# Kernel tuning notes

Measured on AMD Instinct MI355X. Metric: run time of the kernel, lower is better.

Reference implementation:

```python
import jax, jax.numpy as jnp
import numpy as np

DT = 0.01          # oscillator integration step
GPI_TAU = 0.01     # gpi accumulation rate
NOISE_TAU = 1.0    # noise scale
MIN_OMEGA, MAX_OMEGA = 0.1, 1.0


def clinear(xr, xi, Wr, Wi, br, bi):
    # complex linear: (Wr + i Wi)(xr + i xi) + (br + i bi), weights stored [out, in]
    yr = xr @ Wr.T - xi @ Wi.T + br
    yi = xr @ Wi.T + xi @ Wr.T + bi
    return yr, yi


def crelu(yr, yi):
    # ReLU applied to real and imaginary parts independently
    return jax.nn.relu(yr), jax.nn.relu(yi)


def hopf_step(xr, xi, r, phi, omega):
    # Hopf oscillator in polar form, forced by complex input x = xr + i xi:
    #   dr   = dt * ( r(1 - r^2) + Re(x e^{-i phi}) )
    #   dphi = dt * ( omega + Im(x e^{-i phi}) / r )
    # output = r_new * e^{i phi_new}
    c, s = jnp.cos(phi), jnp.sin(phi)
    r_new = r + DT * (r * (1.0 - r * r) + xr * c + xi * s)
    phi_new = phi + DT * (omega + (xi * c - xr * s) / jnp.maximum(r, 1e-6))
    return r_new * jnp.cos(phi_new), r_new * jnp.sin(phi_new), r_new, phi_new


def setup_inputs() -> dict:
    T, D, U, A = 4096, 256, 2048, 64
    key = jax.random.key(0)
    ks = jax.random.split(key, 16)

    def lin(k, out_d, in_d):
        k1, k2, k3, k4 = jax.random.split(k, 4)
        sc = 1.0 / np.sqrt(in_d)
        return (jax.random.normal(k1, (out_d, in_d), dtype=jnp.float32) * sc,
                jax.random.normal(k2, (out_d, in_d), dtype=jnp.float32) * sc,
                jax.random.normal(k3, (out_d,), dtype=jnp.float32) * sc,
                jax.random.normal(k4, (out_d,), dtype=jnp.float32) * sc)

    l1Wr, l1Wi, l1br, l1bi = lin(ks[0], U, D)
    dpWr, dpWi, dpbr, dpbi = lin(ks[1], A, U)
    ipWr, ipWi, ipbr, ipbi = lin(ks[2], A, U)
    cWr, cWi, cbr, cbi = lin(ks[3], 1, U)
    return {
        'state': jax.random.normal(ks[4], (T, 1, D), dtype=jnp.float32),
        'phi1_init': jax.random.uniform(ks[5], (1, U), dtype=jnp.float32),
        'phi2_init': jax.random.uniform(ks[6], (1, U), dtype=jnp.float32),
        'noise_u': jax.random.uniform(ks[7], (T, A), dtype=jnp.float32),
        'omega1': jax.random.uniform(ks[8], (U,), minval=MIN_OMEGA, maxval=MAX_OMEGA, dtype=jnp.float32),
        'omega2': jax.random.uniform(ks[9], (U,), minval=MIN_OMEGA, maxval=MAX_OMEGA, dtype=jnp.float32),
        'l1Wr': l1Wr, 'l1Wi': l1Wi, 'l1br': l1br, 'l1bi': l1bi,
        'dpWr': dpWr, 'dpWi': dpWi, 'dpbr': dpbr, 'dpbi': dpbi,
        'ipWr': ipWr, 'ipWi': ipWi, 'ipbr': ipbr, 'ipbi': ipbi,
        'cWr': cWr, 'cWi': cWi, 'cbr': cbr, 'cbi': cbi,
    }


def reference(state, phi1_init, phi2_init, noise_u, omega1, omega2,
              l1Wr, l1Wi, l1br, l1bi, dpWr, dpWi, dpbr, dpbi,
              ipWr, ipWi, ipbr, ipbi, cWr, cWi, cbr, cbi):
    U = l1Wr.shape[0]
    A = dpWr.shape[0]
    carry0 = (jnp.ones((1, U)), phi1_init * 0.1,   # r1, phi1 (torch.rand/10)
              jnp.ones((1, U)), phi2_init * 0.1,   # r2, phi2
              jnp.zeros((1, A)),                   # gpi
              jnp.zeros((1, 1)))                   # p_value

    def step(carry, xs):
        r1, phi1, r2, phi2, gpi, p_value = carry
        s_t, nz_t = xs  # s_t: [1, D], nz_t: [A]
        # x = cReLU(l1(complex(state[t], state[t])))
        xr, xi = crelu(*clinear(s_t, s_t, l1Wr, l1Wi, l1br, l1bi))
        d1r, d1i, r1, phi1 = hopf_step(xr, xi, r1, phi1, omega1)
        d2r, d2i, r2, phi2 = hopf_step(xr, xi, r2, phi2, omega2)
        vr, vi = clinear(d1r, d1i, cWr, cWi, cbr, cbi)
        value = jnp.sqrt(vr * vr + vi * vi)          # |critic(d1out)|  [1,1]
        delta_V = value - p_value                    # pd_flag = sc_flag = 0
        lD1 = jax.nn.sigmoid(5.0 * delta_V)
        lD2 = jax.nn.sigmoid(-5.0 * delta_V)
        dpr, dpi = crelu(*clinear(d1r * lD1, d1i * lD1, dpWr, dpWi, dpbr, dpbi))
        ipr, ipi = crelu(*clinear(d2r * lD2, d2i * lD2, ipWr, ipWi, ipbr, ipbi))
        noise = NOISE_TAU * (nz_t[None, :] * 2.0 * lD2 - lD2)  # real-valued, adds to real part
        diff_r = dpr - (ipr + noise)
        diff_i = dpi - ipi
        gpi = gpi + GPI_TAU * jnp.sqrt(diff_r * diff_r + diff_i * diff_i)
        return (r1, phi1, r2, phi2, gpi, value), (gpi, value)

    (r1, phi1, r2, phi2, gpi, value), (gpi_traj, value_traj) = jax.lax.scan(
        step, carry0, (state, noise_u))
    probs = jax.nn.softmax(gpi, axis=1)
    return probs, value, gpi_traj
```

## Files before the change

kernel.cpp:

```cpp
#include <hip/hip_runtime.h>
#include <hip/hip_bf16.h>
#include <stdint.h>


#define T_ 4096
#define D_ 256
#define U_ 2048
#define A_ 64

__device__ __forceinline__ uint32_t pack2(float lo, float hi) {
  __hip_bfloat16 l = __float2bfloat16(lo);
  __hip_bfloat16 h = __float2bfloat16(hi);
  uint16_t lu, hu;
  __builtin_memcpy(&lu, &l, 2);
  __builtin_memcpy(&hu, &h, 2);
  return (uint32_t)lu | ((uint32_t)hu << 16);
}
__device__ __forceinline__ float bflo(uint32_t p) { return __uint_as_float(p << 16); }
__device__ __forceinline__ float bfhi(uint32_t p) { return __uint_as_float(p & 0xffff0000u); }

__global__ __launch_bounds__(256) void k_gemm1(
    const float* __restrict__ S, const float* __restrict__ Wr,
    const float* __restrict__ Wi, const float* __restrict__ br,
    const float* __restrict__ bi, float* __restrict__ xc) {
  __shared__ float sT[32][68];
  __shared__ float wrT[32][68];
  __shared__ float wiT[32][68];
  const int tid = threadIdx.x;
  const int t0 = blockIdx.x * 64;
  const int u0 = blockIdx.y * 64;
  const int un = tid & 15, tm = tid >> 4;
  const int lr = tid >> 3;
  const int lc = (tid & 7) * 4;
  float accR[4][4] = {}, accI[4][4] = {};
  for (int k0 = 0; k0 < D_; k0 += 32) {
    __syncthreads();
#pragma unroll
    for (int p = 0; p < 2; ++p) {
      const int row = p * 32 + lr;
      float4 v = *(const float4*)&S[(size_t)(t0 + row) * D_ + k0 + lc];
      sT[lc + 0][row] = v.x; sT[lc + 1][row] = v.y;
      sT[lc + 2][row] = v.z; sT[lc + 3][row] = v.w;
      float4 a = *(const float4*)&Wr[(size_t)(u0 + row) * D_ + k0 + lc];
      wrT[lc + 0][row] = a.x; wrT[lc + 1][row] = a.y;
      wrT[lc + 2][row] = a.z; wrT[lc + 3][row] = a.w;
      float4 b = *(const float4*)&Wi[(size_t)(u0 + row) * D_ + k0 + lc];
      wiT[lc + 0][row] = b.x; wiT[lc + 1][row] = b.y;
      wiT[lc + 2][row] = b.z; wiT[lc + 3][row] = b.w;
    }
    __syncthreads();
#pragma unroll
    for (int k = 0; k < 32; ++k) {
      const float4 sv = *(const float4*)&sT[k][tm * 4];
      const float4 ar = *(const float4*)&wrT[k][un * 4];
      const float4 ai = *(const float4*)&wiT[k][un * 4];
      const float ss[4] = {sv.x, sv.y, sv.z, sv.w};
      const float wd[4] = {ar.x - ai.x, ar.y - ai.y, ar.z - ai.z, ar.w - ai.w};
      const float wm[4] = {ar.x + ai.x, ar.y + ai.y, ar.z + ai.z, ar.w + ai.w};
#pragma unroll
      for (int i = 0; i < 4; ++i)
#pragma unroll
        for (int j = 0; j < 4; ++j) {
          accR[i][j] = fmaf(ss[i], wd[j], accR[i][j]);
          accI[i][j] = fmaf(ss[i], wm[j], accI[i][j]);
        }
    }
  }
  const float4 brv = *(const float4*)&br[u0 + un * 4];
  const float4 biv = *(const float4*)&bi[u0 + un * 4];
  const float brx[4] = {brv.x, brv.y, brv.z, brv.w};
  const float bix[4] = {biv.x, biv.y, biv.z, biv.w};
#pragma unroll
  for (int i = 0; i < 4; ++i) {
    float vr[4], vi[4];
#pragma unroll
    for (int j = 0; j < 4; ++j) {
      vr[j] = fmaxf(accR[i][j] + brx[j], 0.f);
      vi[j] = fmaxf(accI[i][j] + bix[j], 0.f);
    }
    const size_t base = ((size_t)(t0 + tm * 4 + i) * U_ + u0 + un * 4) * 2;
    *(float4*)&xc[base + 0] = make_float4(vr[0], vi[0], vr[1], vi[1]);
    *(float4*)&xc[base + 4] = make_float4(vr[2], vi[2], vr[3], vi[3]);
  }
}

#define HOPF_LOAD(BUF, i, tbase)                                            \
  do {                                                                      \
    const float* bx_ = xc + (size_t)((tbase) + (i)) * (U_ * 2);             \
    asm volatile("global_load_dwordx2 %0, %1, %2"                           \
                 : "=v"(BUF[i])                                             \
                 : "v"(voffx), "s"(bx_));                                   \
  } while (0)

#define HOPF_STEP(BUF, i, tb)                                               \
  do {                                                                      \
    const float xr_ = BUF[i].x, xi_ = BUF[i].y;                             \
    const float f_ = fmaf(xr_, c, xi_ * s);                                 \
    const float g_ = fmaf(xi_, c, -(xr_ * s));                              \
    const float rn_ = fmaf(0.01f, fmaf(r, fmaf(-r, r, 1.0f), f_), r);       \
    const float rinv_ = __builtin_amdgcn_rcpf(fmaxf(r, 1e-6f));             \
    const float phin_ = fmaf(0.01f, g_ * rinv_, phi + dto);                 \
    float cn_, sn_;                                                         \
    __sincosf(phin_, &sn_, &cn_);                                           \
    uint32_t pk_;                                                           \
    asm("v_cvt_pk_bf16_f32 %0, %1, %2"                                     \
        : "=v"(pk_)                                                         \
        : "v"(rn_ * cn_), "v"(rn_ * sn_));                                  \
    const uint32_t* bd_ = dst + (size_t)((tb) + (i)) * U_;                  \
    asm volatile("global_store_dword %0, %1, %2" ::"v"(voffd), "v"(pk_),    \
                 "s"(bd_));                                                  \
    r = rn_; phi = phin_; c = cn_; s = sn_;                                 \
  } while (0)

#define VMWAIT(N)                                  \
  asm volatile("s_waitcnt vmcnt(" #N ")");         \
  __builtin_amdgcn_sched_barrier(0)

__global__ __launch_bounds__(64, 1) void k_hopf(
    const float* __restrict__ xc, const float* __restrict__ phi1,
    const float* __restrict__ phi2, const float* __restrict__ om1,
    const float* __restrict__ om2, uint32_t* __restrict__ d1c,
    uint32_t* __restrict__ d2c) {
  const int ub = blockIdx.x & 31;
  const int osc = blockIdx.x >> 5;
  const int u = ub * 64 + threadIdx.x;
  float phi = (osc ? phi2[u] : phi1[u]) * 0.1f;
  const float omega = osc ? om2[u] : om1[u];
  const uint32_t* __restrict__ dst = (osc ? d2c : d1c);
  const float dto = 0.01f * omega;
  float r = 1.0f;
  float c, s;
  __sincosf(phi, &s, &c);
  const uint32_t voffx = (uint32_t)u * 8u;
  const uint32_t voffd = (uint32_t)u * 4u;

  constexpr int PF = 32;
  float2 bufA[PF], bufB[PF];
#pragma unroll
  for (int i = 0; i < PF; ++i) HOPF_LOAD(bufA, i, 0);
#pragma unroll
  for (int i = 0; i < PF; ++i) HOPF_LOAD(bufB, i, PF);
  VMWAIT(32);

  for (int t0 = 0; t0 < T_; t0 += 2 * PF) {
#pragma unroll
    for (int i = 0; i < PF; ++i) HOPF_STEP(bufA, i, t0);
    {
      int tp = t0 + 2 * PF;
      if (tp >= T_) tp = 0;
#pragma unroll
      for (int i = 0; i < PF; ++i) HOPF_LOAD(bufA, i, tp);
    }
    VMWAIT(63);
#pragma unroll
    for (int i = 0; i < PF; ++i) HOPF_STEP(bufB, i, t0 + PF);
    {
      int tp = t0 + 3 * PF;
      if (tp >= T_) tp = 0;
#pragma unroll
      for (int i = 0; i < PF; ++i) HOPF_LOAD(bufB, i, tp);
    }
    VMWAIT(63);
  }
  asm volatile("s_waitcnt vmcnt(0)");
}

__global__ __launch_bounds__(256) void k_critic(
    const uint32_t* __restrict__ d1c, const float* __restrict__ cWr,
    const float* __restrict__ cWi, const float* __restrict__ cbr,
    const float* __restrict__ cbi, float* __restrict__ value) {
  const int t = blockIdx.x;
  const int tid = threadIdx.x;
  float vr = 0.f, vi = 0.f;
#pragma unroll
  for (int i = 0; i < 8; ++i) {
    const int uu = i * 256 + tid;
    const uint32_t p = d1c[(size_t)t * U_ + uu];
    const float dr = bflo(p), di = bfhi(p);
    const float wr = cWr[uu], wi = cWi[uu];
    vr = fmaf(dr, wr, fmaf(-di, wi, vr));
    vi = fmaf(dr, wi, fmaf(di, wr, vi));
  }
#pragma unroll
  for (int o = 32; o >= 1; o >>= 1) {
    vr += __shfl_xor(vr, o);
    vi += __shfl_xor(vi, o);
  }
  __shared__ float red[2][4];
  if ((tid & 63) == 0) { red[0][tid >> 6] = vr; red[1][tid >> 6] = vi; }
  __syncthreads();
  if (tid == 0) {
    const float r0 = red[0][0] + red[0][1] + red[0][2] + red[0][3] + cbr[0];
    const float i0 = red[1][0] + red[1][1] + red[1][2] + red[1][3] + cbi[0];
    value[t] = sqrtf(r0 * r0 + i0 * i0);
  }
}

__global__ __launch_bounds__(256) void k_ld(const float* __restrict__ value,
                                            float* __restrict__ lD1,
                                            float* __restrict__ lD2) {
  const int t = blockIdx.x * 256 + threadIdx.x;
  const float v = value[t];
  const float pv = (t > 0) ? value[t - 1] : 0.f;
  const float x = 5.0f * (v - pv);
  const float sg = 1.0f / (1.0f + __expf(-x));
  lD1[t] = sg;
  lD2[t] = 1.0f - sg;
}

__global__ __launch_bounds__(256) void k_gemmD(
    const uint32_t* __restrict__ d1c, const uint32_t* __restrict__ d2c,
    const float* __restrict__ dpWr, const float* __restrict__ dpWi,
    const float* __restrict__ ipWr, const float* __restrict__ ipWi,
    float* __restrict__ mpart) {
  __shared__ uint32_t d1T[32][68];
  __shared__ uint32_t d2T[32][68];
  __shared__ float w1r[32][68], w1i[32][68], w2r[32][68], w2i[32][68];
  const int tid = threadIdx.x;
  const int t0 = blockIdx.x * 64;
  const int ks = blockIdx.y;
  const int kb = ks * 512;
  const int an = tid & 15, tm = tid >> 4;
  const int lr = tid >> 3, lc = (tid & 7) * 4;
  float a1r[4][4] = {}, a1i[4][4] = {}, a2r[4][4] = {}, a2i[4][4] = {};
  for (int kc = 0; kc < 512; kc += 32) {
    __syncthreads();
#pragma unroll
    for (int p = 0; p < 2; ++p) {
      const int row = p * 32 + lr;
      const int col = kb + kc + lc;
      uint4 v1 = *(const uint4*)&d1c[(size_t)(t0 + row) * U_ + col];
      d1T[lc + 0][row] = v1.x; d1T[lc + 1][row] = v1.y;
      d1T[lc + 2][row] = v1.z; d1T[lc + 3][row] = v1.w;
      uint4 v2 = *(const uint4*)&d2c[(size_t)(t0 + row) * U_ + col];
      d2T[lc + 0][row] = v2.x; d2T[lc + 1][row] = v2.y;
      d2T[lc + 2][row] = v2.z; d2T[lc + 3][row] = v2.w;
      float4 f;
      f = *(const float4*)&dpWr[(size_t)row * U_ + col];
      w1r[lc + 0][row] = f.x; w1r[lc + 1][row] = f.y;
      w1r[lc + 2][row] = f.z; w1r[lc + 3][row] = f.w;
      f = *(const float4*)&dpWi[(size_t)row * U_ + col];
      w1i[lc + 0][row] = f.x; w1i[lc + 1][row] = f.y;
      w1i[lc + 2][row] = f.z; w1i[lc + 3][row] = f.w;
      f = *(const float4*)&ipWr[(size_t)row * U_ + col];
      w2r[lc + 0][row] = f.x; w2r[lc + 1][row] = f.y;
      w2r[lc + 2][row] = f.z; w2r[lc + 3][row] = f.w;
      f = *(const float4*)&ipWi[(size_t)row * U_ + col];
      w2i[lc + 0][row] = f.x; w2i[lc + 1][row] = f.y;
      w2i[lc + 2][row] = f.z; w2i[lc + 3][row] = f.w;
    }
    __syncthreads();
#pragma unroll
    for (int k = 0; k < 32; ++k) {
      const uint4 p1 = *(const uint4*)&d1T[k][tm * 4];
      const uint4 p2 = *(const uint4*)&d2T[k][tm * 4];
      const float4 q1r = *(const float4*)&w1r[k][an * 4];
      const float4 q1i = *(const float4*)&w1i[k][an * 4];
      const float4 q2r = *(const float4*)&w2r[k][an * 4];
      const float4 q2i = *(const float4*)&w2i[k][an * 4];
      const float d1r_[4] = {bflo(p1.x), bflo(p1.y), bflo(p1.z), bflo(p1.w)};
      const float d1i_[4] = {bfhi(p1.x), bfhi(p1.y), bfhi(p1.z), bfhi(p1.w)};
      const float d2r_[4] = {bflo(p2.x), bflo(p2.y), bflo(p2.z), bflo(p2.w)};
      const float d2i_[4] = {bfhi(p2.x), bfhi(p2.y), bfhi(p2.z), bfhi(p2.w)};
      const float u1r[4] = {q1r.x, q1r.y, q1r.z, q1r.w};
      const float u1i[4] = {q1i.x, q1i.y, q1i.z, q1i.w};
      const float u2r[4] = {q2r.x, q2r.y, q2r.z, q2r.w};
      const float u2i[4] = {q2i.x, q2i.y, q2i.z, q2i.w};
#pragma unroll
      for (int i = 0; i < 4; ++i)
#pragma unroll
        for (int j = 0; j < 4; ++j) {
          a1r[i][j] = fmaf(d1r_[i], u1r[j], fmaf(-d1i_[i], u1i[j], a1r[i][j]));
          a1i[i][j] = fmaf(d1r_[i], u1i[j], fmaf(d1i_[i], u1r[j], a1i[i][j]));
          a2r[i][j] = fmaf(d2r_[i], u2r[j], fmaf(-d2i_[i], u2i[j], a2r[i][j]));
          a2i[i][j] = fmaf(d2r_[i], u2i[j], fmaf(d2i_[i], u2r[j], a2i[i][j]));
        }
    }
  }
  const size_t MS = (size_t)T_ * A_;
#pragma unroll
  for (int i = 0; i < 4; ++i) {
    const size_t base = (size_t)(t0 + tm * 4 + i) * A_ + an * 4;
    *(float4*)&mpart[(size_t)(0 * 4 + ks) * MS + base] =
        make_float4(a1r[i][0], a1r[i][1], a1r[i][2], a1r[i][3]);
    *(float4*)&mpart[(size_t)(1 * 4 + ks) * MS + base] =
        make_float4(a1i[i][0], a1i[i][1], a1i[i][2], a1i[i][3]);
    *(float4*)&mpart[(size_t)(2 * 4 + ks) * MS + base] =
        make_float4(a2r[i][0], a2r[i][1], a2r[i][2], a2r[i][3]);
    *(float4*)&mpart[(size_t)(3 * 4 + ks) * MS + base] =
        make_float4(a2i[i][0], a2i[i][1], a2i[i][2], a2i[i][3]);
  }
}

__global__ __launch_bounds__(256) void k_epi(
    const float* __restrict__ mpart, const float* __restrict__ lD1,
    const float* __restrict__ lD2, const float* __restrict__ noise,
    const float* __restrict__ dpbr, const float* __restrict__ dpbi,
    const float* __restrict__ ipbr, const float* __restrict__ ipbi,
    float* __restrict__ nrm) {
  const size_t MS = (size_t)T_ * A_;
  const int gid = blockIdx.x * 256 + threadIdx.x;
  const size_t e0 = (size_t)gid * 4;
  const int t = (int)(e0 >> 6);
  const int a0 = (int)(e0 & 63);
  float m[4][4];
#pragma unroll
  for (int mi = 0; mi < 4; ++mi) {
    float4 acc = *(const float4*)&mpart[(size_t)(mi * 4 + 0) * MS + e0];
#pragma unroll
    for (int ksi = 1; ksi < 4; ++ksi) {
      const float4 v = *(const float4*)&mpart[(size_t)(mi * 4 + ksi) * MS + e0];
      acc.x += v.x; acc.y += v.y; acc.z += v.z; acc.w += v.w;
    }
    m[mi][0] = acc.x; m[mi][1] = acc.y; m[mi][2] = acc.z; m[mi][3] = acc.w;
  }
  const float l1 = lD1[t], l2 = lD2[t];
  const float4 nzv = *(const float4*)&noise[e0];
  const float nz[4] = {nzv.x, nzv.y, nzv.z, nzv.w};
  const float4 q1 = *(const float4*)&dpbr[a0];
  const float4 q2 = *(const float4*)&dpbi[a0];
  const float4 q3 = *(const float4*)&ipbr[a0];
  const float4 q4 = *(const float4*)&ipbi[a0];
  const float b1r[4] = {q1.x, q1.y, q1.z, q1.w};
  const float b1i[4] = {q2.x, q2.y, q2.z, q2.w};
  const float b2r[4] = {q3.x, q3.y, q3.z, q3.w};
  const float b2i[4] = {q4.x, q4.y, q4.z, q4.w};
  float res[4];
#pragma unroll
  for (int j = 0; j < 4; ++j) {
    const float dpr = fmaxf(fmaf(l1, m[0][j], b1r[j]), 0.f);
    const float dpi = fmaxf(fmaf(l1, m[1][j], b1i[j]), 0.f);
    const float ipr = fmaxf(fmaf(l2, m[2][j], b2r[j]), 0.f);
    const float ipi = fmaxf(fmaf(l2, m[3][j], b2i[j]), 0.f);
    const float nzs = l2 * (2.f * nz[j] - 1.f);
    const float dr = dpr - ipr - nzs;
    const float di = dpi - ipi;
    res[j] = sqrtf(dr * dr + di * di);
  }
  *(float4*)&nrm[e0] = make_float4(res[0], res[1], res[2], res[3]);
}

__global__ __launch_bounds__(64) void k_scan_part(const float* __restrict__ nrm,
                                                  float* __restrict__ csum) {
  const int c = blockIdx.x;
  const int a = threadIdx.x;
  const int tb = c * 64;
  float run = 0.f;
  for (int i = 0; i < 64; ++i) run += nrm[(size_t)(tb + i) * 64 + a];
  csum[c * 64 + a] = run;
}

__global__ __launch_bounds__(64) void k_scan_mid(const float* __restrict__ csum,
                                                 const float* __restrict__ value,
                                                 float* __restrict__ coff,
                                                 float* __restrict__ out) {
  const int a = threadIdx.x;
  float acc = 0.f;
#pragma unroll
  for (int cc = 0; cc < 64; ++cc) {
    coff[cc * 64 + a] = acc;
    acc += csum[cc * 64 + a];
  }
  const float g = 0.01f * acc;
  float mx = g;
#pragma unroll
  for (int o = 32; o >= 1; o >>= 1) mx = fmaxf(mx, __shfl_xor(mx, o));
  const float e = __expf(g - mx);
  float sm = e;
#pragma unroll
  for (int o = 32; o >= 1; o >>= 1) sm += __shfl_xor(sm, o);
  out[a] = e / sm;
  if (a == 0) out[64] = value[T_ - 1];
}

__global__ __launch_bounds__(64) void k_scan_out(const float* __restrict__ nrm,
                                                 const float* __restrict__ coff,
                                                 float* __restrict__ out) {
  const int c = blockIdx.x;
  const int a = threadIdx.x;
  const int tb = c * 64;
  float off = coff[c * 64 + a];
  float* o65 = out + 65;
  for (int i = 0; i < 64; ++i) {
    off += nrm[(size_t)(tb + i) * 64 + a];
    o65[(size_t)(tb + i) * 64 + a] = 0.01f * off;
  }
}

extern "C" void kernel_launch(void* const* d_in, const int* in_sizes, int n_in,
                              void* d_out, int out_size, void* d_ws,
                              size_t ws_size, hipStream_t stream) {
  const float* state = (const float*)d_in[0];
  const float* phi1 = (const float*)d_in[1];
  const float* phi2 = (const float*)d_in[2];
  const float* noise = (const float*)d_in[3];
  const float* om1 = (const float*)d_in[4];
  const float* om2 = (const float*)d_in[5];
  const float* l1Wr = (const float*)d_in[6];
  const float* l1Wi = (const float*)d_in[7];
  const float* l1br = (const float*)d_in[8];
  const float* l1bi = (const float*)d_in[9];
  const float* dpWr = (const float*)d_in[10];
  const float* dpWi = (const float*)d_in[11];
  const float* dpbr = (const float*)d_in[12];
  const float* dpbi = (const float*)d_in[13];
  const float* ipWr = (const float*)d_in[14];
  const float* ipWi = (const float*)d_in[15];
  const float* ipbr = (const float*)d_in[16];
  const float* ipbi = (const float*)d_in[17];
  const float* cWr = (const float*)d_in[18];
  const float* cWi = (const float*)d_in[19];
  const float* cbr = (const float*)d_in[20];
  const float* cbi = (const float*)d_in[21];
  float* out = (float*)d_out;

  char* ws = (char*)d_ws;
  float* xc = (float*)(ws + (size_t)0);
  uint32_t* d1c = (uint32_t*)(ws + (size_t)67108864);
  uint32_t* d2c = (uint32_t*)(ws + (size_t)100663296);
  float* mpart = (float*)(ws + (size_t)0);
  float* nrm = (float*)(ws + (size_t)16777216);
  float* value = (float*)(ws + (size_t)17825792);
  float* lD1 = (float*)(ws + (size_t)17825792 + 16384);
  float* lD2 = (float*)(ws + (size_t)17825792 + 32768);
  float* csum = (float*)(ws + (size_t)17825792 + 49152);
  float* coff = (float*)(ws + (size_t)17825792 + 65536);

  k_gemm1<<<dim3(T_ / 64, U_ / 64), 256, 0, stream>>>(state, l1Wr, l1Wi, l1br,
                                                      l1bi, xc);
  k_hopf<<<64, 64, 0, stream>>>(xc, phi1, phi2, om1, om2, d1c, d2c);
  k_critic<<<T_, 256, 0, stream>>>(d1c, cWr, cWi, cbr, cbi, value);
  k_ld<<<T_ / 256, 256, 0, stream>>>(value, lD1, lD2);
  k_gemmD<<<dim3(T_ / 64, 4), 256, 0, stream>>>(d1c, d2c, dpWr, dpWi, ipWr,
                                                ipWi, mpart);
  k_epi<<<256, 256, 0, stream>>>(mpart, lD1, lD2, noise, dpbr, dpbi, ipbr,
                                 ipbi, nrm);
  k_scan_part<<<64, 64, 0, stream>>>(nrm, csum);
  k_scan_mid<<<1, 64, 0, stream>>>(csum, value, coff, out);
  k_scan_out<<<64, 64, 0, stream>>>(nrm, coff, out);
}
```

Before: 576.5 us.

## Fuse first complex GEMM with Hopf scan using per-tile ready flags

```diff
diff --git a/kernel.cpp b/kernel.cpp
--- a/kernel.cpp
+++ b/kernel.cpp
@@ -18,71 +18,6 @@
 }
 __device__ __forceinline__ float bflo(uint32_t p) { return __uint_as_float(p << 16); }
 __device__ __forceinline__ float bfhi(uint32_t p) { return __uint_as_float(p & 0xffff0000u); }
-
-__global__ __launch_bounds__(256) void k_gemm1(
-    const float* __restrict__ S, const float* __restrict__ Wr,
-    const float* __restrict__ Wi, const float* __restrict__ br,
-    const float* __restrict__ bi, float* __restrict__ xc) {
-  __shared__ float sT[32][68];
-  __shared__ float wrT[32][68];
-  __shared__ float wiT[32][68];
-  const int tid = threadIdx.x;
-  const int t0 = blockIdx.x * 64;
-  const int u0 = blockIdx.y * 64;
-  const int un = tid & 15, tm = tid >> 4;
-  const int lr = tid >> 3;
-  const int lc = (tid & 7) * 4;
-  float accR[4][4] = {}, accI[4][4] = {};
-  for (int k0 = 0; k0 < D_; k0 += 32) {
-    __syncthreads();
-#pragma unroll
-    for (int p = 0; p < 2; ++p) {
-      const int row = p * 32 + lr;
-      float4 v = *(const float4*)&S[(size_t)(t0 + row) * D_ + k0 + lc];
-      sT[lc + 0][row] = v.x; sT[lc + 1][row] = v.y;
-      sT[lc + 2][row] = v.z; sT[lc + 3][row] = v.w;
-      float4 a = *(const float4*)&Wr[(size_t)(u0 + row) * D_ + k0 + lc];
-      wrT[lc + 0][row] = a.x; wrT[lc + 1][row] = a.y;
-      wrT[lc + 2][row] = a.z; wrT[lc + 3][row] = a.w;
-      float4 b = *(const float4*)&Wi[(size_t)(u0 + row) * D_ + k0 + lc];
-      wiT[lc + 0][row] = b.x; wiT[lc + 1][row] = b.y;
-      wiT[lc + 2][row] = b.z; wiT[lc + 3][row] = b.w;
-    }
-    __syncthreads();
-#pragma unroll
-    for (int k = 0; k < 32; ++k) {
-      const float4 sv = *(const float4*)&sT[k][tm * 4];
-      const float4 ar = *(const float4*)&wrT[k][un * 4];
-      const float4 ai = *(const float4*)&wiT[k][un * 4];
-      const float ss[4] = {sv.x, sv.y, sv.z, sv.w};
-      const float wd[4] = {ar.x - ai.x, ar.y - ai.y, ar.z - ai.z, ar.w - ai.w};
-      const float wm[4] = {ar.x + ai.x, ar.y + ai.y, ar.z + ai.z, ar.w + ai.w};
-#pragma unroll
-      for (int i = 0; i < 4; ++i)
-#pragma unroll
-        for (int j = 0; j < 4; ++j) {
-          accR[i][j] = fmaf(ss[i], wd[j], accR[i][j]);
-          accI[i][j] = fmaf(ss[i], wm[j], accI[i][j]);
-        }
-    }
-  }
-  const float4 brv = *(const float4*)&br[u0 + un * 4];
-  const float4 biv = *(const float4*)&bi[u0 + un * 4];
-  const float brx[4] = {brv.x, brv.y, brv.z, brv.w};
-  const float bix[4] = {biv.x, biv.y, biv.z, biv.w};
-#pragma unroll
-  for (int i = 0; i < 4; ++i) {
-    float vr[4], vi[4];
-#pragma unroll
-    for (int j = 0; j < 4; ++j) {
-      vr[j] = fmaxf(accR[i][j] + brx[j], 0.f);
-      vi[j] = fmaxf(accI[i][j] + bix[j], 0.f);
-    }
-    const size_t base = ((size_t)(t0 + tm * 4 + i) * U_ + u0 + un * 4) * 2;
-    *(float4*)&xc[base + 0] = make_float4(vr[0], vi[0], vr[1], vi[1]);
-    *(float4*)&xc[base + 4] = make_float4(vr[2], vi[2], vr[3], vi[3]);
-  }
-}
 
 #define HOPF_LOAD(BUF, i, tbase)                                            \
   do {                                                                      \
@@ -116,13 +51,94 @@
   asm volatile("s_waitcnt vmcnt(" #N ")");         \
   __builtin_amdgcn_sched_barrier(0)
 
-__global__ __launch_bounds__(64, 1) void k_hopf(
-    const float* __restrict__ xc, const float* __restrict__ phi1,
+#define WAIT_TILE(tt)                                                       \
+  do {                                                                      \
+    while (__hip_atomic_load(&flags[tt], __ATOMIC_ACQUIRE,                  \
+                             __HIP_MEMORY_SCOPE_AGENT) < 32u)               \
+      __builtin_amdgcn_s_sleep(2);                                          \
+    __builtin_amdgcn_sched_barrier(0);                                      \
+  } while (0)
+
+__global__ __launch_bounds__(256) void k_g1hopf(
+    const float* __restrict__ S, const float* __restrict__ Wr,
+    const float* __restrict__ Wi, const float* __restrict__ br,
+    const float* __restrict__ bi, const float* __restrict__ phi1,
     const float* __restrict__ phi2, const float* __restrict__ om1,
-    const float* __restrict__ om2, uint32_t* __restrict__ d1c,
-    uint32_t* __restrict__ d2c) {
-  const int ub = blockIdx.x & 31;
-  const int osc = blockIdx.x >> 5;
+    const float* __restrict__ om2, float* __restrict__ xc,
+    uint32_t* __restrict__ d1c, uint32_t* __restrict__ d2c,
+    uint32_t* __restrict__ flags) {
+  const int bid = blockIdx.x;
+  if (bid >= 64) {
+    __shared__ float sT[32][68];
+    __shared__ float wrT[32][68];
+    __shared__ float wiT[32][68];
+    const int tid = threadIdx.x;
+    const int gb = bid - 64;
+    const int t0 = (gb >> 5) * 64;
+    const int u0 = (gb & 31) * 64;
+    const int un = tid & 15, tm = tid >> 4;
+    const int lr = tid >> 3;
+    const int lc = (tid & 7) * 4;
+    float accR[4][4] = {}, accI[4][4] = {};
+    for (int k0 = 0; k0 < D_; k0 += 32) {
+      __syncthreads();
+#pragma unroll
+      for (int p = 0; p < 2; ++p) {
+        const int row = p * 32 + lr;
+        float4 v = *(const float4*)&S[(size_t)(t0 + row) * D_ + k0 + lc];
+        sT[lc + 0][row] = v.x; sT[lc + 1][row] = v.y;
+        sT[lc + 2][row] = v.z; sT[lc + 3][row] = v.w;
+        float4 a = *(const float4*)&Wr[(size_t)(u0 + row) * D_ + k0 + lc];
+        wrT[lc + 0][row] = a.x; wrT[lc + 1][row] = a.y;
+        wrT[lc + 2][row] = a.z; wrT[lc + 3][row] = a.w;
+        float4 b = *(const float4*)&Wi[(size_t)(u0 + row) * D_ + k0 + lc];
+        wiT[lc + 0][row] = b.x; wiT[lc + 1][row] = b.y;
+        wiT[lc + 2][row] = b.z; wiT[lc + 3][row] = b.w;
+      }
+      __syncthreads();
+#pragma unroll
+      for (int k = 0; k < 32; ++k) {
+        const float4 sv = *(const float4*)&sT[k][tm * 4];
+        const float4 ar = *(const float4*)&wrT[k][un * 4];
+        const float4 ai = *(const float4*)&wiT[k][un * 4];
+        const float ss[4] = {sv.x, sv.y, sv.z, sv.w};
+        const float wd[4] = {ar.x - ai.x, ar.y - ai.y, ar.z - ai.z, ar.w - ai.w};
+        const float wm[4] = {ar.x + ai.x, ar.y + ai.y, ar.z + ai.z, ar.w + ai.w};
+#pragma unroll
+        for (int i = 0; i < 4; ++i)
+#pragma unroll
+          for (int j = 0; j < 4; ++j) {
+            accR[i][j] = fmaf(ss[i], wd[j], accR[i][j]);
+            accI[i][j] = fmaf(ss[i], wm[j], accI[i][j]);
+          }
+      }
+    }
+    const float4 brv = *(const float4*)&br[u0 + un * 4];
+    const float4 biv = *(const float4*)&bi[u0 + un * 4];
+    const float brx[4] = {brv.x, brv.y, brv.z, brv.w};
+    const float bix[4] = {biv.x, biv.y, biv.z, biv.w};
+#pragma unroll
+    for (int i = 0; i < 4; ++i) {
+      float vr[4], vi[4];
+#pragma unroll
+      for (int j = 0; j < 4; ++j) {
+        vr[j] = fmaxf(accR[i][j] + brx[j], 0.f);
+        vi[j] = fmaxf(accI[i][j] + bix[j], 0.f);
+      }
+      const size_t base = ((size_t)(t0 + tm * 4 + i) * U_ + u0 + un * 4) * 2;
+      *(float4*)&xc[base + 0] = make_float4(vr[0], vi[0], vr[1], vi[1]);
+      *(float4*)&xc[base + 4] = make_float4(vr[2], vi[2], vr[3], vi[3]);
+    }
+    __threadfence();
+    __syncthreads();
+    if (tid == 0)
+      __hip_atomic_fetch_add(&flags[t0 >> 6], 1u, __ATOMIC_RELEASE,
+                             __HIP_MEMORY_SCOPE_AGENT);
+    return;
+  }
+  if (threadIdx.x >= 64) return;
+  const int ub = bid & 31;
+  const int osc = bid >> 5;
   const int u = ub * 64 + threadIdx.x;
   float phi = (osc ? phi2[u] : phi1[u]) * 0.1f;
   const float omega = osc ? om2[u] : om1[u];
@@ -136,6 +152,7 @@
 
   constexpr int PF = 32;
   float2 bufA[PF], bufB[PF];
+  WAIT_TILE(0);
 #pragma unroll
   for (int i = 0; i < PF; ++i) HOPF_LOAD(bufA, i, 0);
 #pragma unroll
@@ -148,6 +165,7 @@
     {
       int tp = t0 + 2 * PF;
       if (tp >= T_) tp = 0;
+      WAIT_TILE(tp >> 6);
 #pragma unroll
       for (int i = 0; i < PF; ++i) HOPF_LOAD(bufA, i, tp);
     }
@@ -425,10 +443,12 @@
   float* lD2 = (float*)(ws + (size_t)17825792 + 32768);
   float* csum = (float*)(ws + (size_t)17825792 + 49152);
   float* coff = (float*)(ws + (size_t)17825792 + 65536);
-
-  k_gemm1<<<dim3(T_ / 64, U_ / 64), 256, 0, stream>>>(state, l1Wr, l1Wi, l1br,
-                                                      l1bi, xc);
-  k_hopf<<<64, 64, 0, stream>>>(xc, phi1, phi2, om1, om2, d1c, d2c);
+  uint32_t* flags = (uint32_t*)out;
+
+  hipMemsetAsync(out, 0, 256, stream);
+  k_g1hopf<<<64 + (T_ / 64) * (U_ / 64), 256, 0, stream>>>(
+      state, l1Wr, l1Wi, l1br, l1bi, phi1, phi2, om1, om2, xc, d1c, d2c,
+      flags);
   k_critic<<<T_, 256, 0, stream>>>(d1c, cWr, cWi, cbr, cbi, value);
   k_ld<<<T_ / 256, 256, 0, stream>>>(value, lD1, lD2);
   k_gemmD<<<dim3(T_ / 64, 4), 256, 0, stream>>>(d1c, d2c, dpWr, dpWi, ipWr,
```

After: 769.8 us. 1.34x slower.
